# Optimization experiments

Measured on AMD Instinct MI355X. Metric: run time of the kernel, lower is better.

Reference implementation:

```python
import jax, jax.numpy as jnp
import numpy as np

B, L = 2, 2048          # batch, seq len (self-attention: M == L)
H, D, NB = 8, 16, 8     # n_heads, clifford_dim, n_blades (2^3 for sig_g=[1,1,1])
DM = H * D * NB         # d_model = 1024

# reverse() signs per blade for a 3D algebra, blade grades [0,1,1,1,2,2,2,3]:
# (-1)^{k(k-1)/2}; Euclidean metric signs from get_blade_signs are all +1,
# so the combined twist q_w = reverse(q) * signs is just these per-blade signs.
REV_SIGNS = jnp.array([1., 1., 1., 1., -1., -1., -1., -1.], dtype=jnp.float32)


def setup_inputs() -> dict:
    key = jax.random.key(0)
    ks = jax.random.split(key, 7)
    s = 1.0 / np.sqrt(DM)
    return {
        "query": jax.random.normal(ks[0], (B, L, DM), dtype=jnp.float32),
        "Wq": jax.random.normal(ks[1], (DM, DM), dtype=jnp.float32) * s,
        "bq": jax.random.normal(ks[2], (DM,), dtype=jnp.float32) * s,
        "Wk": jax.random.normal(ks[3], (DM, DM), dtype=jnp.float32) * s,
        "bk": jax.random.normal(ks[4], (DM,), dtype=jnp.float32) * s,
        "Wv": jax.random.normal(ks[5], (DM, DM), dtype=jnp.float32) * s,
        "bv": jax.random.normal(ks[6], (DM,), dtype=jnp.float32) * s,
    }


def reference(query, Wq, bq, Wk, bk, Wv, bv):
    b, l, _ = query.shape
    # projections (torch Linear: x @ W^T + b), reshape to (B,H,L,D,NB)
    def proj(x, W, bias):
        y = x @ W.T + bias
        return y.reshape(b, l, H, D, NB).transpose(0, 2, 1, 3, 4)

    q = proj(query, Wq, bq)
    k = proj(query, Wk, bk)   # self-attention: key = value = query
    v = proj(query, Wv, bv)

    q_w = q * REV_SIGNS  # reverse + blade-sign twist (elementwise over blade axis)
    scale = 1.0 / np.sqrt(D * NB)
    logits = jnp.einsum('bhldi,bhmdi->bhlm', q_w, k) * scale
    attn = jax.nn.softmax(logits, axis=-1)
    out = jnp.einsum('bhlm,bhmdi->bhldi', attn, v)
    out = out.transpose(0, 2, 1, 3, 4).reshape(b, l, -1)
    return out, attn.mean(axis=1)  # need_weights=True path
```

## Files before the change

### kernel.cpp

```cpp
#include <hip/hip_runtime.h>

typedef __attribute__((ext_vector_type(8))) __bf16 bf16x8;
typedef __attribute__((ext_vector_type(4))) __bf16 bf16x4;
typedef __attribute__((ext_vector_type(4))) float f32x4;
typedef __attribute__((ext_vector_type(16))) float f32x16;
typedef __attribute__((ext_vector_type(8))) unsigned short us8;
typedef __attribute__((ext_vector_type(4))) unsigned int u32x4;

constexpr float SCALE_L2E = 0.08838834764831845f * 1.4426950408889634f;

__device__ __forceinline__ unsigned short f2bf(float f) {
  unsigned int u = __float_as_uint(f);
  u = (u + 0x7FFFu + ((u >> 16) & 1u)) >> 16;
  return (unsigned short)u;
}

__device__ __forceinline__ void gl_lds16(const void* g, void* l) {
  __builtin_amdgcn_global_load_lds(
      (__attribute__((address_space(1))) void*)const_cast<void*>(g),
      (__attribute__((address_space(3))) void*)l, 16, 0, 0);
}

__global__ __launch_bounds__(256) void k_convert(
    const float* __restrict__ q, const float* __restrict__ wq,
    const float* __restrict__ wk, const float* __restrict__ wv,
    unsigned short* __restrict__ xb, unsigned short* __restrict__ wb) {
  long i = ((long)blockIdx.x * 256 + threadIdx.x) * 8;
  const float* s; unsigned short* d;
  if (i < 4194304)      { s = q  + i;             d = xb + i; }
  else if (i < 5242880) { s = wq + (i - 4194304); d = wb + (i - 4194304); }
  else if (i < 6291456) { s = wk + (i - 5242880); d = wb + 1048576 + (i - 5242880); }
  else                  { s = wv + (i - 6291456); d = wb + 2097152 + (i - 6291456); }
  float4 a = *(const float4*)s;
  float4 b = *(const float4*)(s + 4);
  us8 r;
  r[0]=f2bf(a.x); r[1]=f2bf(a.y); r[2]=f2bf(a.z); r[3]=f2bf(a.w);
  r[4]=f2bf(b.x); r[5]=f2bf(b.y); r[6]=f2bf(b.z); r[7]=f2bf(b.w);
  *(us8*)d = r;
}

__global__ __launch_bounds__(256) void k_proj(
    const unsigned short* __restrict__ xb, const unsigned short* __restrict__ wb,
    const float* __restrict__ bq, const float* __restrict__ bk, const float* __restrict__ bv,
    unsigned short* __restrict__ oq, unsigned short* __restrict__ ok_, unsigned short* __restrict__ vt) {
  __shared__ unsigned short As[4096];
  __shared__ unsigned short Bs[4096];
  const int t = threadIdx.x;
  const int wave = t >> 6, lane = t & 63;
  const int lrow = lane & 15, grp = lane >> 4;
  const int z = blockIdx.z;
  const unsigned short* w = wb + (size_t)z * 1048576;
  const float* bias = (z == 0) ? bq : ((z == 1) ? bk : bv);

  const unsigned short* asrc = xb + ((size_t)(blockIdx.y * 128 + (t >> 2)) * 1024 + (t & 3) * 8);
  const unsigned short* bsrc = w  + ((size_t)(blockIdx.x * 128 + (t >> 2)) * 1024 + (t & 3) * 8);

  f32x4 acc[4][4] = {};
  for (int kt = 0; kt < 32; ++kt) {
    gl_lds16(asrc + kt*32,              &As[t*8]);
    gl_lds16(asrc + kt*32 + 64*1024,    &As[2048 + t*8]);
    gl_lds16(bsrc + kt*32,              &Bs[t*8]);
    gl_lds16(bsrc + kt*32 + 64*1024,    &Bs[2048 + t*8]);
    __syncthreads();
    const int wr = wave >> 1, wc = wave & 1;
    bf16x8 af[4], bf[4];
#pragma unroll
    for (int mf = 0; mf < 4; ++mf)
      af[mf] = *(const bf16x8*)&As[(wr*64 + mf*16 + lrow)*32 + grp*8];
#pragma unroll
    for (int nf = 0; nf < 4; ++nf)
      bf[nf] = *(const bf16x8*)&Bs[(wc*64 + nf*16 + lrow)*32 + grp*8];
#pragma unroll
    for (int mf = 0; mf < 4; ++mf)
#pragma unroll
      for (int nf = 0; nf < 4; ++nf)
        acc[mf][nf] = __builtin_amdgcn_mfma_f32_16x16x32_bf16(af[mf], bf[nf], acc[mf][nf], 0, 0, 0);
    __syncthreads();
  }
  const int wr = wave >> 1, wc = wave & 1;
  if (z == 2) {
#pragma unroll
    for (int nf = 0; nf < 4; ++nf) {
      const int col = blockIdx.x*128 + wc*64 + nf*16 + lrow;
      const int h = col >> 7, dd = col & 127;
      const int dt = dd >> 5, lv = dd & 31;
      const float bsv = bias[col];
#pragma unroll
      for (int mf = 0; mf < 4; ++mf) {
        const int r0 = blockIdx.y*128 + wr*64 + mf*16 + grp*4;
        const int bb = r0 >> 11, m = r0 & 2047;
        const int mc = m >> 4, him = (m >> 3) & 1, j0 = m & 7;
        bf16x4 pv;
#pragma unroll
        for (int i = 0; i < 4; ++i) pv[i] = (__bf16)(acc[mf][nf][i] + bsv);
        const size_t off = ((((size_t)((bb*8 + h)*4 + dt))*128 + mc)*64 + lv + 32*him)*8 + j0;
        *(bf16x4*)&vt[off] = pv;
      }
    }
  } else {
    unsigned short* dst = (z == 0) ? oq : ok_;
    const float sign = (z == 0 && (lane & 7) >= 4) ? -1.0f : 1.0f;
#pragma unroll
    for (int nf = 0; nf < 4; ++nf) {
      const int col = blockIdx.x*128 + wc*64 + nf*16 + lrow;
      const float bsv = bias[col];
#pragma unroll
      for (int mf = 0; mf < 4; ++mf)
#pragma unroll
        for (int i = 0; i < 4; ++i) {
          const int row = blockIdx.y*128 + wr*64 + mf*16 + grp*4 + i;
          dst[(size_t)row*1024 + col] = f2bf((acc[mf][nf][i] + bsv) * sign);
        }
    }
  }
}

__global__ __launch_bounds__(256) void k_repack(const unsigned short* __restrict__ kws,
                                                unsigned short* __restrict__ kfrag) {
  const int c = blockIdx.x * 256 + threadIdx.x;
  const int lane = c & 63, kc = (c >> 6) & 7, mtile = (c >> 9) & 63, bh = c >> 15;
  const int b = bh >> 3, h = bh & 7;
  const int m = mtile*32 + (lane & 31);
  const int kd = kc*16 + (lane >> 5)*8;
  us8 v = *(const us8*)&kws[((size_t)(b*2048 + m))*1024 + h*128 + kd];
  *(us8*)&kfrag[(size_t)c * 8] = v;
}

__global__ __launch_bounds__(512) void k_attn_out(
    const unsigned short* __restrict__ qw, const unsigned short* __restrict__ kfrag,
    const unsigned short* __restrict__ vfrag, float* __restrict__ outp,
    float* __restrict__ rsw) {
  __shared__ unsigned short KsL[2][8192];
  __shared__ unsigned short VsL[2][8192];
  __shared__ float slab[8][32][36];
  __shared__ float rsred[8][32];
  __shared__ float invb[128];

  const int bid = blockIdx.x;
  const int xcd = bid & 7, r_ = bid >> 3;
  const int bh = (xcd << 1) | (r_ & 1);
  const int lt = r_ >> 1;
  const int b = bh >> 3, h = bh & 7;
  const int t = threadIdx.x;
  const int wave = t >> 6, lane = t & 63;
  const int mg = wave >> 2, lg = wave & 3;
  const int lm = lane & 31, hi = lane >> 5;

  bf16x8 qf[8];
  {
    const unsigned short* qp = qw + ((size_t)(b*2048 + lt*128 + lg*32 + lm))*1024
                                  + (size_t)h*128 + hi*8;
#pragma unroll
    for (int kc = 0; kc < 8; ++kc) qf[kc] = *(const bf16x8*)(qp + kc*16);
  }

  const unsigned short* kbp = kfrag + (size_t)bh*262144;
  const unsigned short* vbp = vfrag + (size_t)bh*262144;

  const int vdt = (t >> 6) & 3, vw2 = (t >> 8) & 1, vi8 = (t & 63) * 8;

  auto STAGE = [&](int buf, int it) {
#pragma unroll
    for (int q = 0; q < 2; ++q)
      gl_lds16(kbp + (q*32 + it)*4096 + t*8, &KsL[buf][q*4096 + t*8]);
#pragma unroll
    for (int r = 0; r < 2; ++r)
      gl_lds16(vbp + vdt*65536 + (r*64 + it*2 + vw2)*512 + vi8, &VsL[buf][r*4096 + t*8]);
  };

  f32x16 oacc[4] = {};
  float rs = 0.f;

  STAGE(0, 0);
  __syncthreads();

  for (int it = 0; it < 32; ++it) {
    const int cur = it & 1;
    if (it + 1 < 32) STAGE(cur ^ 1, it + 1);

    bf16x8 kf[8];
#pragma unroll
    for (int kc = 0; kc < 8; ++kc)
      kf[kc] = *(const bf16x8*)&KsL[cur][mg*4096 + kc*512 + lane*8];
    f32x16 s = {};
#pragma unroll
    for (int kc = 0; kc < 8; ++kc)
      s = __builtin_amdgcn_mfma_f32_32x32x16_bf16(kf[kc], qf[kc], s, 0, 0, 0);

    bf16x8 vf[8];
#pragma unroll
    for (int w2 = 0; w2 < 2; ++w2)
#pragma unroll
      for (int dt = 0; dt < 4; ++dt)
        vf[w2*4 + dt] = *(const bf16x8*)&VsL[cur][(mg*8 + w2*4 + dt)*512 + lane*8];

    float e[16];
#pragma unroll
    for (int r = 0; r < 16; ++r) e[r] = __builtin_amdgcn_exp2f(s[r] * SCALE_L2E);
    float ps = 0.f;
#pragma unroll
    for (int r = 0; r < 16; ++r) ps += e[r];
    rs += ps;

    bf16x8 pf[2];
#pragma unroll
    for (int w2 = 0; w2 < 2; ++w2) {
      unsigned a0, a1, b0, b1;
      asm("v_cvt_pk_bf16_f32 %0, %1, %2" : "=v"(a0) : "v"(e[8*w2+0]), "v"(e[8*w2+1]));
      asm("v_cvt_pk_bf16_f32 %0, %1, %2" : "=v"(a1) : "v"(e[8*w2+2]), "v"(e[8*w2+3]));
      asm("v_cvt_pk_bf16_f32 %0, %1, %2" : "=v"(b0) : "v"(e[8*w2+4]), "v"(e[8*w2+5]));
      asm("v_cvt_pk_bf16_f32 %0, %1, %2" : "=v"(b1) : "v"(e[8*w2+6]), "v"(e[8*w2+7]));
      asm("v_permlane32_swap_b32 %0, %1" : "+v"(a0), "+v"(b0));
      asm("v_permlane32_swap_b32 %0, %1" : "+v"(a1), "+v"(b1));
      u32x4 pw = {a0, a1, b0, b1};
      pf[w2] = __builtin_bit_cast(bf16x8, pw);
    }

#pragma unroll
    for (int dt = 0; dt < 4; ++dt) {
      oacc[dt] = __builtin_amdgcn_mfma_f32_32x32x16_bf16(vf[dt],     pf[0], oacc[dt], 0, 0, 0);
      oacc[dt] = __builtin_amdgcn_mfma_f32_32x32x16_bf16(vf[4 + dt], pf[1], oacc[dt], 0, 0, 0);
    }
    __syncthreads();
  }

  rs += __shfl_xor(rs, 32, 64);
  if (lane < 32) rsred[wave][lm] = rs;
  __syncthreads();
  if (t < 128) {
    const int tlg = t >> 5, tl = t & 31;
    const float tot = rsred[tlg][tl] + rsred[4 + tlg][tl];
    rsw[(size_t)bh*2048 + lt*128 + t] = tot;
    invb[t] = 1.0f / tot;
  }

#pragma unroll
  for (int dt = 0; dt < 4; ++dt) {
    __syncthreads();
#pragma unroll
    for (int c = 0; c < 4; ++c) {
      float4 v4 = { oacc[dt][4*c + 0], oacc[dt][4*c + 1], oacc[dt][4*c + 2], oacc[dt][4*c + 3] };
      *(float4*)&slab[wave][lm][8*c + 4*hi] = v4;
    }
    __syncthreads();
    const int tlg = t >> 7, idx = t & 127;
    const int l = idx >> 2, d0 = (idx & 3) * 8;
    const float iv = invb[tlg*32 + l];
    float4 x0 = *(const float4*)&slab[tlg][l][d0];
    float4 x1 = *(const float4*)&slab[tlg][l][d0 + 4];
    float4 y0 = *(const float4*)&slab[4 + tlg][l][d0];
    float4 y1 = *(const float4*)&slab[4 + tlg][l][d0 + 4];
    float4 o0 = { (x0.x + y0.x)*iv, (x0.y + y0.y)*iv, (x0.z + y0.z)*iv, (x0.w + y0.w)*iv };
    float4 o1 = { (x1.x + y1.x)*iv, (x1.y + y1.y)*iv, (x1.z + y1.z)*iv, (x1.w + y1.w)*iv };
    float* op = outp + ((size_t)(b*2048 + lt*128 + tlg*32 + l))*1024 + h*128 + dt*32 + d0;
    *(float4*)op = o0;
    *(float4*)(op + 4) = o1;
  }
}

__global__ __launch_bounds__(256) void k_attn_mean(
    const unsigned short* __restrict__ qw, const unsigned short* __restrict__ kb,
    const float* __restrict__ rsw, float* __restrict__ meanp) {
  __shared__ unsigned short Qs[128*128];
  __shared__ unsigned short Ks[128*128];
  __shared__ float inv_s[8*128];
  const int mt = blockIdx.x;
  const int lt = blockIdx.y;
  const int b  = blockIdx.z;
  const int t = threadIdx.x;
  const int wave = t >> 6, lane = t & 63;
  const int lrow = lane & 15, grp = lane >> 4;
  const int wl = wave >> 1, wm = wave & 1;
  const int trow = t >> 4;
  const int tcol = t & 15;

  for (int idx = t; idx < 1024; idx += 256) {
    int hh = idx >> 7, ll = idx & 127;
    inv_s[idx] = 1.0f / rsw[(size_t)(b*8 + hh)*2048 + lt*128 + ll];
  }

  f32x4 acc[4][4] = {};

  for (int h = 0; h < 8; ++h) {
    __syncthreads();
    const unsigned short* qbase = qw + ((size_t)(b*2048 + lt*128) * 1024 + h*128);
    const unsigned short* kbase = kb + ((size_t)(b*2048 + mt*128) * 1024 + h*128);
#pragma unroll
    for (int i = 0; i < 8; ++i) {
      const int row = i*16 + trow;
      const int sc = (tcol ^ (row & 7)) * 8;
      gl_lds16(qbase + (size_t)row*1024 + sc, &Qs[i*2048 + t*8]);
      gl_lds16(kbase + (size_t)row*1024 + sc, &Ks[i*2048 + t*8]);
    }
    __syncthreads();

    f32x4 s[4][4] = {};
#pragma unroll
    for (int ks = 0; ks < 4; ++ks) {
      bf16x8 af[4], bf[4];
#pragma unroll
      for (int lf = 0; lf < 4; ++lf) {
        const int row = wl*64 + lf*16 + lrow;
        af[lf] = *(const bf16x8*)&Qs[row*128 + ((ks*32 + grp*8) ^ ((row & 7) << 3))];
      }
#pragma unroll
      for (int mf = 0; mf < 4; ++mf) {
        const int row = wm*64 + mf*16 + lrow;
        bf[mf] = *(const bf16x8*)&Ks[row*128 + ((ks*32 + grp*8) ^ ((row & 7) << 3))];
      }
#pragma unroll
      for (int lf = 0; lf < 4; ++lf)
#pragma unroll
        for (int mf = 0; mf < 4; ++mf)
          s[lf][mf] = __builtin_amdgcn_mfma_f32_16x16x32_bf16(af[lf], bf[mf], s[lf][mf], 0, 0, 0);
    }
#pragma unroll
    for (int lf = 0; lf < 4; ++lf)
#pragma unroll
      for (int i = 0; i < 4; ++i) {
        const float iv = inv_s[h*128 + wl*64 + lf*16 + grp*4 + i];
#pragma unroll
        for (int mf = 0; mf < 4; ++mf)
          acc[lf][mf][i] += __builtin_amdgcn_exp2f(s[lf][mf][i] * SCALE_L2E) * iv;
      }
  }

#pragma unroll
  for (int lf = 0; lf < 4; ++lf)
#pragma unroll
    for (int i = 0; i < 4; ++i) {
      const int l = lt*128 + wl*64 + lf*16 + grp*4 + i;
      const size_t rowo = (size_t)(b*2048 + l) * 2048;
#pragma unroll
      for (int mf = 0; mf < 4; ++mf)
        meanp[rowo + mt*128 + wm*64 + mf*16 + lrow] = acc[lf][mf][i] * 0.125f;
    }
}

extern "C" void kernel_launch(void* const* d_in, const int* in_sizes, int n_in,
                              void* d_out, int out_size, void* d_ws, size_t ws_size,
                              hipStream_t stream) {
  (void)in_sizes; (void)n_in; (void)out_size; (void)ws_size;
  const float* query = (const float*)d_in[0];
  const float* Wq = (const float*)d_in[1];
  const float* bq = (const float*)d_in[2];
  const float* Wk = (const float*)d_in[3];
  const float* bk = (const float*)d_in[4];
  const float* Wv = (const float*)d_in[5];
  const float* bv = (const float*)d_in[6];
  float* outp  = (float*)d_out;
  float* meanp = outp + 4194304;

  char* ws = (char*)d_ws;
  unsigned short* xb    = (unsigned short*)(ws);
  unsigned short* wb    = (unsigned short*)(ws + 8388608);
  unsigned short* qws   = (unsigned short*)(ws + 14680064);
  unsigned short* kws   = (unsigned short*)(ws + 23068672);
  unsigned short* kfrag = (unsigned short*)(ws + 31457280);
  unsigned short* vfrag = (unsigned short*)(ws + 39845888);
  float*          rsw   = (float*)(ws + 48234496);

  k_convert<<<3584, 256, 0, stream>>>(query, Wq, Wk, Wv, xb, wb);
  k_proj<<<dim3(8, 32, 3), 256, 0, stream>>>(xb, wb, bq, bk, bv, qws, kws, vfrag);
  k_repack<<<2048, 256, 0, stream>>>(kws, kfrag);
  k_attn_out<<<256, 512, 0, stream>>>(qws, kfrag, vfrag, outp, rsw);
  k_attn_mean<<<dim3(16, 16, 2), 256, 0, stream>>>(qws, kws, rsw, meanp);
}
```

Baseline: 138.1 us.

## Halve attention query tile to 64 rows, run 512 blocks of 256 threads

The attention-output kernel now handles 64 query rows per block with 4 waves instead of 128 rows with 8 waves, and the grid doubles to 512 blocks. Each thread issues twice as many global-to-LDS loads for the K/V stages, and the shared-memory buffers are merged into one 64KB pool that the epilogue slab reuses. The aim is more blocks to fill all CUs on the MI355X, since 256 blocks fall short of the CU count. The cost is twice the total K/V traffic, because each block still streams the full key sequence for only half as many query rows.

```diff
diff --git a/kernel.cpp b/kernel.cpp
--- a/kernel.cpp
+++ b/kernel.cpp
@@ -126,15 +126,16 @@
   *(us8*)&kfrag[(size_t)c * 8] = v;
 }
 
-__global__ __launch_bounds__(512) void k_attn_out(
+__global__ __launch_bounds__(256) void k_attn_out(
     const unsigned short* __restrict__ qw, const unsigned short* __restrict__ kfrag,
     const unsigned short* __restrict__ vfrag, float* __restrict__ outp,
     float* __restrict__ rsw) {
-  __shared__ unsigned short KsL[2][8192];
-  __shared__ unsigned short VsL[2][8192];
-  __shared__ float slab[8][32][36];
-  __shared__ float rsred[8][32];
-  __shared__ float invb[128];
+  __shared__ __align__(16) char pool[65536];
+  unsigned short (*KsL)[8192] = (unsigned short(*)[8192])pool;
+  unsigned short (*VsL)[8192] = (unsigned short(*)[8192])(pool + 32768);
+  float (*slab)[32][36] = (float(*)[32][36])pool;
+  float (*rsred)[32] = (float(*)[32])(pool + 61440);
+  float* invb = (float*)(pool + 62464);
 
   const int bid = blockIdx.x;
   const int xcd = bid & 7, r_ = bid >> 3;
@@ -143,12 +144,12 @@
   const int b = bh >> 3, h = bh & 7;
   const int t = threadIdx.x;
   const int wave = t >> 6, lane = t & 63;
-  const int mg = wave >> 2, lg = wave & 3;
+  const int mg = wave >> 1, lg = wave & 1;
   const int lm = lane & 31, hi = lane >> 5;
 
   bf16x8 qf[8];
   {
-    const unsigned short* qp = qw + ((size_t)(b*2048 + lt*128 + lg*32 + lm))*1024
+    const unsigned short* qp = qw + ((size_t)(b*2048 + lt*64 + lg*32 + lm))*1024
                                   + (size_t)h*128 + hi*8;
 #pragma unroll
     for (int kc = 0; kc < 8; ++kc) qf[kc] = *(const bf16x8*)(qp + kc*16);
@@ -156,16 +157,20 @@
 
   const unsigned short* kbp = kfrag + (size_t)bh*262144;
   const unsigned short* vbp = vfrag + (size_t)bh*262144;
-
-  const int vdt = (t >> 6) & 3, vw2 = (t >> 8) & 1, vi8 = (t & 63) * 8;
+  const int vdt = (t >> 6) & 3, vln = (t & 63) * 8;
 
   auto STAGE = [&](int buf, int it) {
 #pragma unroll
     for (int q = 0; q < 2; ++q)
-      gl_lds16(kbp + (q*32 + it)*4096 + t*8, &KsL[buf][q*4096 + t*8]);
-#pragma unroll
-    for (int r = 0; r < 2; ++r)
-      gl_lds16(vbp + vdt*65536 + (r*64 + it*2 + vw2)*512 + vi8, &VsL[buf][r*4096 + t*8]);
+#pragma unroll
+      for (int p = 0; p < 2; ++p)
+        gl_lds16(kbp + (q*32 + it)*4096 + (p*256 + t)*8, &KsL[buf][q*4096 + (p*256 + t)*8]);
+#pragma unroll
+    for (int s = 0; s < 2; ++s)
+#pragma unroll
+      for (int w2 = 0; w2 < 2; ++w2)
+        gl_lds16(vbp + vdt*65536 + (s*64 + it*2 + w2)*512 + vln,
+                 &VsL[buf][s*4096 + w2*2048 + vdt*512 + vln]);
   };
 
   f32x16 oacc[4] = {};
@@ -192,7 +197,7 @@
     for (int w2 = 0; w2 < 2; ++w2)
 #pragma unroll
       for (int dt = 0; dt < 4; ++dt)
-        vf[w2*4 + dt] = *(const bf16x8*)&VsL[cur][(mg*8 + w2*4 + dt)*512 + lane*8];
+        vf[w2*4 + dt] = *(const bf16x8*)&VsL[cur][mg*4096 + w2*2048 + dt*512 + lane*8];
 
     float e[16];
 #pragma unroll
@@ -227,10 +232,10 @@
   rs += __shfl_xor(rs, 32, 64);
   if (lane < 32) rsred[wave][lm] = rs;
   __syncthreads();
-  if (t < 128) {
+  if (t < 64) {
     const int tlg = t >> 5, tl = t & 31;
-    const float tot = rsred[tlg][tl] + rsred[4 + tlg][tl];
-    rsw[(size_t)bh*2048 + lt*128 + t] = tot;
+    const float tot = rsred[tlg][tl] + rsred[2 + tlg][tl];
+    rsw[(size_t)bh*2048 + lt*64 + t] = tot;
     invb[t] = 1.0f / tot;
   }
 
@@ -243,16 +248,16 @@
       *(float4*)&slab[wave][lm][8*c + 4*hi] = v4;
     }
     __syncthreads();
-    const int tlg = t >> 7, idx = t & 127;
+    const int lgg = t >> 7, idx = t & 127;
     const int l = idx >> 2, d0 = (idx & 3) * 8;
-    const float iv = invb[tlg*32 + l];
-    float4 x0 = *(const float4*)&slab[tlg][l][d0];
-    float4 x1 = *(const float4*)&slab[tlg][l][d0 + 4];
-    float4 y0 = *(const float4*)&slab[4 + tlg][l][d0];
-    float4 y1 = *(const float4*)&slab[4 + tlg][l][d0 + 4];
+    const float iv = invb[lgg*32 + l];
+    float4 x0 = *(const float4*)&slab[lgg][l][d0];
+    float4 x1 = *(const float4*)&slab[lgg][l][d0 + 4];
+    float4 y0 = *(const float4*)&slab[2 + lgg][l][d0];
+    float4 y1 = *(const float4*)&slab[2 + lgg][l][d0 + 4];
     float4 o0 = { (x0.x + y0.x)*iv, (x0.y + y0.y)*iv, (x0.z + y0.z)*iv, (x0.w + y0.w)*iv };
     float4 o1 = { (x1.x + y1.x)*iv, (x1.y + y1.y)*iv, (x1.z + y1.z)*iv, (x1.w + y1.w)*iv };
-    float* op = outp + ((size_t)(b*2048 + lt*128 + tlg*32 + l))*1024 + h*128 + dt*32 + d0;
+    float* op = outp + ((size_t)(b*2048 + lt*64 + lgg*32 + l))*1024 + h*128 + dt*32 + d0;
     *(float4*)op = o0;
     *(float4*)(op + 4) = o1;
   }
@@ -363,6 +368,6 @@
   k_convert<<<3584, 256, 0, stream>>>(query, Wq, Wk, Wv, xb, wb);
   k_proj<<<dim3(8, 32, 3), 256, 0, stream>>>(xb, wb, bq, bk, bv, qws, kws, vfrag);
   k_repack<<<2048, 256, 0, stream>>>(kws, kfrag);
-  k_attn_out<<<256, 512, 0, stream>>>(qws, kfrag, vfrag, outp, rsw);
+  k_attn_out<<<512, 256, 0, stream>>>(qws, kfrag, vfrag, outp, rsw);
   k_attn_mean<<<dim3(16, 16, 2), 256, 0, stream>>>(qws, kws, rsw, meanp);
 }
```

Measured after the change: 136.7 us. About the same (-1.1%).

## Rewrite attention-mean kernel to read MFMA-fragment layouts directly without LDS

Applied to the files above, without the earlier changes.

The attention-mean kernel now loads pre-repacked Q and K fragments straight from global memory into registers and uses 32x32x16 MFMAs, so the LDS staging and its barriers per head are gone. Blocks are remapped so that each XCD works on its own set of tiles. An extra repack launch builds the Q fragment buffer, and the attn_out shared arrays are merged into one aliased pool to cut LDS use. The cost is one more kernel launch and extra memory traffic, and the new mean kernel may rely more on the L2 cache because it no longer reuses tiles through LDS.

```diff
diff --git a/kernel.cpp b/kernel.cpp
--- a/kernel.cpp
+++ b/kernel.cpp
@@ -115,26 +115,27 @@
   }
 }
 
-__global__ __launch_bounds__(256) void k_repack(const unsigned short* __restrict__ kws,
-                                                unsigned short* __restrict__ kfrag) {
+__global__ __launch_bounds__(256) void k_repack(const unsigned short* __restrict__ src,
+                                                unsigned short* __restrict__ frag) {
   const int c = blockIdx.x * 256 + threadIdx.x;
   const int lane = c & 63, kc = (c >> 6) & 7, mtile = (c >> 9) & 63, bh = c >> 15;
   const int b = bh >> 3, h = bh & 7;
   const int m = mtile*32 + (lane & 31);
   const int kd = kc*16 + (lane >> 5)*8;
-  us8 v = *(const us8*)&kws[((size_t)(b*2048 + m))*1024 + h*128 + kd];
-  *(us8*)&kfrag[(size_t)c * 8] = v;
+  us8 v = *(const us8*)&src[((size_t)(b*2048 + m))*1024 + h*128 + kd];
+  *(us8*)&frag[(size_t)c * 8] = v;
 }
 
 __global__ __launch_bounds__(512) void k_attn_out(
     const unsigned short* __restrict__ qw, const unsigned short* __restrict__ kfrag,
     const unsigned short* __restrict__ vfrag, float* __restrict__ outp,
     float* __restrict__ rsw) {
-  __shared__ unsigned short KsL[2][8192];
-  __shared__ unsigned short VsL[2][8192];
-  __shared__ float slab[8][32][36];
-  __shared__ float rsred[8][32];
-  __shared__ float invb[128];
+  __shared__ __align__(16) char pool[65536];
+  unsigned short (*KsL)[8192] = (unsigned short(*)[8192])pool;
+  unsigned short (*VsL)[8192] = (unsigned short(*)[8192])(pool + 32768);
+  float (*slab)[32][36] = (float(*)[32][36])pool;
+  float (*rsred)[32] = (float(*)[32])(pool + 40960);
+  float* invb = (float*)(pool + 45056);
 
   const int bid = blockIdx.x;
   const int xcd = bid & 7, r_ = bid >> 3;
@@ -156,7 +157,6 @@
 
   const unsigned short* kbp = kfrag + (size_t)bh*262144;
   const unsigned short* vbp = vfrag + (size_t)bh*262144;
-
   const int vdt = (t >> 6) & 3, vw2 = (t >> 8) & 1, vi8 = (t & 63) * 8;
 
   auto STAGE = [&](int buf, int it) {
@@ -259,82 +259,50 @@
 }
 
 __global__ __launch_bounds__(256) void k_attn_mean(
-    const unsigned short* __restrict__ qw, const unsigned short* __restrict__ kb,
+    const unsigned short* __restrict__ qfrag, const unsigned short* __restrict__ kfrag,
     const float* __restrict__ rsw, float* __restrict__ meanp) {
-  __shared__ unsigned short Qs[128*128];
-  __shared__ unsigned short Ks[128*128];
-  __shared__ float inv_s[8*128];
-  const int mt = blockIdx.x;
-  const int lt = blockIdx.y;
-  const int b  = blockIdx.z;
+  __shared__ float inv_s[256];
+  const int u = blockIdx.x;
+  const int xcd = u & 7, s_ = u >> 3;
+  const int mq = xcd*2 + (s_ & 1);
+  const int lt = (s_ >> 1) & 63;
+  const int b  = s_ >> 7;
   const int t = threadIdx.x;
   const int wave = t >> 6, lane = t & 63;
-  const int lrow = lane & 15, grp = lane >> 4;
-  const int wl = wave >> 1, wm = wave & 1;
-  const int trow = t >> 4;
-  const int tcol = t & 15;
-
-  for (int idx = t; idx < 1024; idx += 256) {
-    int hh = idx >> 7, ll = idx & 127;
-    inv_s[idx] = 1.0f / rsw[(size_t)(b*8 + hh)*2048 + lt*128 + ll];
-  }
-
-  f32x4 acc[4][4] = {};
-
+  const int mc = mq*4 + wave;
+  const int lm = lane & 31, hi = lane >> 5;
+
+  inv_s[t] = 1.0f / rsw[(size_t)(b*8 + (t >> 5))*2048 + lt*32 + (t & 31)];
+  __syncthreads();
+
+  float acc[16] = {};
   for (int h = 0; h < 8; ++h) {
-    __syncthreads();
-    const unsigned short* qbase = qw + ((size_t)(b*2048 + lt*128) * 1024 + h*128);
-    const unsigned short* kbase = kb + ((size_t)(b*2048 + mt*128) * 1024 + h*128);
-#pragma unroll
-    for (int i = 0; i < 8; ++i) {
-      const int row = i*16 + trow;
-      const int sc = (tcol ^ (row & 7)) * 8;
-      gl_lds16(qbase + (size_t)row*1024 + sc, &Qs[i*2048 + t*8]);
-      gl_lds16(kbase + (size_t)row*1024 + sc, &Ks[i*2048 + t*8]);
-    }
-    __syncthreads();
-
-    f32x4 s[4][4] = {};
-#pragma unroll
-    for (int ks = 0; ks < 4; ++ks) {
-      bf16x8 af[4], bf[4];
-#pragma unroll
-      for (int lf = 0; lf < 4; ++lf) {
-        const int row = wl*64 + lf*16 + lrow;
-        af[lf] = *(const bf16x8*)&Qs[row*128 + ((ks*32 + grp*8) ^ ((row & 7) << 3))];
-      }
-#pragma unroll
-      for (int mf = 0; mf < 4; ++mf) {
-        const int row = wm*64 + mf*16 + lrow;
-        bf[mf] = *(const bf16x8*)&Ks[row*128 + ((ks*32 + grp*8) ^ ((row & 7) << 3))];
-      }
-#pragma unroll
-      for (int lf = 0; lf < 4; ++lf)
-#pragma unroll
-        for (int mf = 0; mf < 4; ++mf)
-          s[lf][mf] = __builtin_amdgcn_mfma_f32_16x16x32_bf16(af[lf], bf[mf], s[lf][mf], 0, 0, 0);
-    }
-#pragma unroll
-    for (int lf = 0; lf < 4; ++lf)
-#pragma unroll
-      for (int i = 0; i < 4; ++i) {
-        const float iv = inv_s[h*128 + wl*64 + lf*16 + grp*4 + i];
-#pragma unroll
-        for (int mf = 0; mf < 4; ++mf)
-          acc[lf][mf][i] += __builtin_amdgcn_exp2f(s[lf][mf][i] * SCALE_L2E) * iv;
-      }
-  }
-
-#pragma unroll
-  for (int lf = 0; lf < 4; ++lf)
-#pragma unroll
-    for (int i = 0; i < 4; ++i) {
-      const int l = lt*128 + wl*64 + lf*16 + grp*4 + i;
-      const size_t rowo = (size_t)(b*2048 + l) * 2048;
-#pragma unroll
-      for (int mf = 0; mf < 4; ++mf)
-        meanp[rowo + mt*128 + wm*64 + mf*16 + lrow] = acc[lf][mf][i] * 0.125f;
-    }
+    const int bh = b*8 + h;
+    const unsigned short* qp = qfrag + (size_t)(bh*64 + lt)*4096 + lane*8;
+    const unsigned short* kp = kfrag + (size_t)(bh*64 + mc)*4096 + lane*8;
+    bf16x8 qf[8], kf[8];
+#pragma unroll
+    for (int kc = 0; kc < 8; ++kc) {
+      qf[kc] = *(const bf16x8*)(qp + kc*512);
+      kf[kc] = *(const bf16x8*)(kp + kc*512);
+    }
+    f32x16 s = {};
+#pragma unroll
+    for (int kc = 0; kc < 8; ++kc)
+      s = __builtin_amdgcn_mfma_f32_32x32x16_bf16(qf[kc], kf[kc], s, 0, 0, 0);
+#pragma unroll
+    for (int rq = 0; rq < 4; ++rq) {
+      f32x4 ivq = *(const f32x4*)&inv_s[h*32 + rq*8 + hi*4];
+#pragma unroll
+      for (int j = 0; j < 4; ++j)
+        acc[rq*4 + j] += __builtin_amdgcn_exp2f(s[rq*4 + j] * SCALE_L2E) * ivq[j];
+    }
+  }
+#pragma unroll
+  for (int r = 0; r < 16; ++r) {
+    const int l = lt*32 + (r & 3) + 8*(r >> 2) + 4*hi;
+    meanp[((size_t)(b*2048 + l))*2048 + mc*32 + lm] = acc[r] * 0.125f;
+  }
 }
 
 extern "C" void kernel_launch(void* const* d_in, const int* in_sizes, int n_in,
@@ -359,10 +327,12 @@
   unsigned short* kfrag = (unsigned short*)(ws + 31457280);
   unsigned short* vfrag = (unsigned short*)(ws + 39845888);
   float*          rsw   = (float*)(ws + 48234496);
+  unsigned short* qfrag = (unsigned short*)(ws + 48365568);
 
   k_convert<<<3584, 256, 0, stream>>>(query, Wq, Wk, Wv, xb, wb);
   k_proj<<<dim3(8, 32, 3), 256, 0, stream>>>(xb, wb, bq, bk, bv, qws, kws, vfrag);
   k_repack<<<2048, 256, 0, stream>>>(kws, kfrag);
+  k_repack<<<2048, 256, 0, stream>>>(qws, qfrag);
   k_attn_out<<<256, 512, 0, stream>>>(qws, kfrag, vfrag, outp, rsw);
-  k_attn_mean<<<dim3(16, 16, 2), 256, 0, stream>>>(qws, kws, rsw, meanp);
-}
+  k_attn_mean<<<2048, 256, 0, stream>>>(qfrag, kfrag, rsw, meanp);
+}
```

New measurement: 129.8 us. 1.06x faster.
